# Kernel tuning notes

Measured on AMD Instinct MI355X. Metric: run time of the kernel, lower is better.

## Reference

```python
import jax, jax.numpy as jnp
import numpy as np

B, S, H, DFF, HOP = 64, 512, 512, 2048, 6
THRESHOLD = 1.0 - 0.1  # self.threshold in the torch module


def setup_inputs() -> dict:
    key = jax.random.key(0)
    k = jax.random.split(key, 8)
    sc = 0.02
    return {
        "state": jax.random.normal(k[0], (B, S, H), jnp.float32),
        "inputs": jax.random.normal(k[1], (B, S, H), jnp.float32),
        "time_enc": jax.random.normal(k[2], (1, S, H), jnp.float32) * sc,
        "pos_enc": jax.random.normal(k[3], (1, HOP, H), jnp.float32) * sc,
        "w_p": jax.random.normal(k[4], (H,), jnp.float32) * sc,
        "b_p": jnp.ones((1,), jnp.float32),  # p.bias.data.fill_(1)
        "w1": jax.random.normal(k[5], (H, DFF), jnp.float32) * sc,
        "b1": jnp.zeros((DFF,), jnp.float32),
        "w2": jax.random.normal(k[6], (DFF, H), jnp.float32) * sc,
        "b2": jnp.zeros((H,), jnp.float32),
        "max_hop": HOP,
    }


def reference(state, inputs, time_enc, pos_enc, w_p, b_p, w1, b1, w2, b2, max_hop):
    Bv, Sv, Hv = inputs.shape
    dt = state.dtype
    zeros_bs = jnp.zeros((Bv, Sv), dt)

    def step(carry, pos_t):
        st, halting, remainders, n_updates, prev = carry
        # time + per-step positional signal
        st = st + time_enc[:, :Sv, :] + pos_t[None, None, :]
        # halting probability p = sigmoid(Linear(state)) -> [B,S]
        p = jax.nn.sigmoid(jnp.einsum('bsh,h->bs', st, w_p) + b_p[0])
        still = (halting < 1.0).astype(dt)
        cand = halting + p * still
        new_halted = (cand > THRESHOLD).astype(dt) * still
        still = (cand <= THRESHOLD).astype(dt) * still
        halting = halting + p * still
        remainders = remainders + new_halted * (1.0 - halting)
        halting = halting + new_halted * remainders
        n_updates = n_updates + still + new_halted
        uw = (p * still + new_halted * remainders)[..., None]  # update weights
        # fn(state): wrapped transformer sublayer, here a dense FFN
        st = jnp.maximum(st @ w1 + b1, 0.0) @ w2 + b2
        prev = st * uw + prev * (1.0 - uw)
        return (st, halting, remainders, n_updates, prev), None

    init = (state, zeros_bs, zeros_bs, zeros_bs, jnp.zeros_like(inputs))
    # Fixed max_hop iterations: once a position halts, still/new_halted are 0
    # and all its bookkeeping + blended state are exact no-ops, so this matches
    # the data-dependent torch while-loop exactly.
    (st, halting, remainders, n_updates, prev), _ = jax.lax.scan(
        step, init, pos_enc[0, :max_hop])
    return prev, remainders, n_updates
```

## Files before the change

kernel.cpp:

```cpp
#include <hip/hip_runtime.h>
#include <math.h>

typedef short short8 __attribute__((ext_vector_type(8)));
typedef _Float16 half8 __attribute__((ext_vector_type(8)));
typedef float floatx4 __attribute__((ext_vector_type(4)));

#define Bb 64
#define Ss 512
#define Hh 512
#define DFF 2048
#define HOPS 6
#define BS (Bb*Ss)
#define PS 1048576
#define BUFSZ 16384
#define RSCALE 2048.0f
#define RINV   (1.0f/2048.0f)

__device__ inline unsigned short f16u(float v) {
  _Float16 h = (_Float16)v;
  union { _Float16 h; unsigned short u; } c; c.h = h; return c.u;
}
__device__ inline void split8_store1(const float* xs, unsigned short* dst) {
  unsigned q[4];
#pragma unroll
  for (int j = 0; j < 4; ++j)
    q[j] = (unsigned)f16u(xs[2*j]) | ((unsigned)f16u(xs[2*j+1]) << 16);
  *(int4*)dst = make_int4(q[0], q[1], q[2], q[3]);
}

__device__ __forceinline__ void gload16(const void* g, void* l) {
  __builtin_amdgcn_global_load_lds(
      (const __attribute__((address_space(1))) void*)g,
      (__attribute__((address_space(3))) void*)l, 16, 0, 0);
}

__global__ __launch_bounds__(256) void prep_kernel(
    const float* __restrict__ w, unsigned short* __restrict__ wf,
    int K32, int NTOT, int N)
{
  int id = blockIdx.x * 256 + threadIdx.x;
  if (id >= K32 * NTOT * 64) return;
  int l  = id & 63;
  int NT = (id >> 6) % NTOT;
  int k0 = id / (64 * NTOT);
  int n  = NT * 16 + (l & 15);
  int kb = k0 * 32 + 8 * (l >> 4);
  float xs[8];
#pragma unroll
  for (int j = 0; j < 8; ++j) xs[j] = w[(size_t)(kb + j) * N + n];
  split8_store1(xs, wf + (size_t)id * 8);
}

__global__ __launch_bounds__(1024) void compact_kernel(
    const float* __restrict__ halting, int* __restrict__ idx,
    int* __restrict__ cnt, int tzero)
{
  __shared__ int wsum[16];
  __shared__ int wbase[16];
  __shared__ int s_base;
  int tid = threadIdx.x;
  int lane = tid & 63, wid = tid >> 6;
  int pos = blockIdx.x * 1024 + tid;
  int flag = tzero ? 1 : ((halting[pos] < 1.0f) ? 1 : 0);
  unsigned long long m = __ballot(flag);
  int pre = __popcll(m & ((1ull << lane) - 1ull));
  if (lane == 0) wsum[wid] = __popcll(m);
  __syncthreads();
  if (tid == 0) {
    int a = 0;
#pragma unroll
    for (int i = 0; i < 16; ++i) { wbase[i] = a; a += wsum[i]; }
    s_base = (a > 0) ? atomicAdd(cnt, a) : 0;
  }
  __syncthreads();
  if (flag) idx[s_base + wbase[wid] + pre] = pos;
}

__global__ __launch_bounds__(256) void halt_kernel(
    const float* __restrict__ st, const float* __restrict__ te,
    const float* __restrict__ pe_t, const float* __restrict__ wp,
    const float* __restrict__ bp, float* __restrict__ halting,
    float* __restrict__ remainders, float* __restrict__ n_updates,
    float* __restrict__ uw_c, const int* __restrict__ idxbuf,
    const int* __restrict__ cntp, int tzero)
{
  int cnt = *cntp;
  int i = blockIdx.x * 4 + (threadIdx.x >> 6);
  if (i >= cnt) return;
  int lane = threadIdx.x & 63;
  int pos = idxbuf[i];
  int s = pos & (Ss - 1);
  const float4* stv = (const float4*)(st + (size_t)pos * Hh);
  const float4* tev = (const float4*)(te + (size_t)s * Hh);
  const float4* pev = (const float4*)pe_t;
  const float4* wpv = (const float4*)wp;
  float sum = 0.f;
#pragma unroll
  for (int j = 0; j < 2; ++j) {
    int idx = lane + j * 64;
    float4 a = stv[idx], b = tev[idx], c = pev[idx], w = wpv[idx];
    sum += (a.x + b.x + c.x) * w.x + (a.y + b.y + c.y) * w.y +
           (a.z + b.z + c.z) * w.z + (a.w + b.w + c.w) * w.w;
  }
#pragma unroll
  for (int off = 32; off > 0; off >>= 1) sum += __shfl_xor(sum, off, 64);
  if (lane == 0) {
    float y = sum + bp[0];
    float p = 1.0f / (1.0f + expf(-y));
    const float THRESH = 1.0f - 0.1f;
    float h0  = tzero ? 0.f : halting[pos];
    float rem = tzero ? 0.f : remainders[pos];
    float nup = tzero ? 0.f : n_updates[pos];
    float still = (h0 < 1.0f) ? 1.f : 0.f;
    float cand  = h0 + p * still;
    float nh  = ((cand >  THRESH) ? 1.f : 0.f) * still;
    float st2 = ((cand <= THRESH) ? 1.f : 0.f) * still;
    h0  += p * st2;
    rem += nh * (1.0f - h0);
    h0  += nh * rem;
    nup += st2 + nh;
    float uwv = p * st2 + nh * rem;
    halting[pos]    = h0;
    remainders[pos] = rem;
    n_updates[pos]  = nup;
    uw_c[i]         = uwv;
  }
}

__global__ __launch_bounds__(256) void stagex_kernel(
    const float* __restrict__ st, const float* __restrict__ te,
    const float* __restrict__ pe_t, unsigned short* __restrict__ xf,
    const int* __restrict__ idxbuf, const int* __restrict__ cntp,
    int m_base, int mrows)
{
  const int K32 = Hh / 32;
  int cnt = *cntp;
  int rel = cnt - m_base;
  if (rel <= 0) return;
  if (rel > mrows) rel = mrows;
  int rows_pad = (rel + 127) & ~127;
  if (rows_pad > mrows) rows_pad = mrows;
  int id = blockIdx.x * 256 + threadIdx.x;
  int l = id & 63;
  int f = id >> 6;
  int mtile = f / K32, k0 = f - mtile * K32;
  if (mtile * 16 >= rows_pad) return;
  int m = m_base + mtile * 16 + (l & 15);
  int mc = (m < cnt) ? m : cnt - 1;
  int pos = idxbuf[mc];
  int kb = k0 * 32 + (l >> 4) * 8;
  const float* ap = st + (size_t)pos * Hh + kb;
  const float* tp = te + (size_t)(pos & (Ss - 1)) * Hh + kb;
  const float* pp = pe_t + kb;
  float4 xa = *(const float4*)ap, xb = *(const float4*)(ap + 4);
  float4 ta = *(const float4*)tp, tb = *(const float4*)(tp + 4);
  float4 pa = *(const float4*)pp, pb = *(const float4*)(pp + 4);
  float xs[8];
  xs[0] = xa.x + ta.x + pa.x; xs[1] = xa.y + ta.y + pa.y;
  xs[2] = xa.z + ta.z + pa.z; xs[3] = xa.w + ta.w + pa.w;
  xs[4] = xb.x + tb.x + pb.x; xs[5] = xb.y + tb.y + pb.y;
  xs[6] = xb.z + tb.z + pb.z; xs[7] = xb.w + tb.w + pb.w;
  split8_store1(xs, xf + ((size_t)f * 64 + l) * 8);
}


#define LSTR 66
__global__ __launch_bounds__(256, 2) void gemm1_kernel(
    const unsigned short* __restrict__ xf, const unsigned short* __restrict__ w1f,
    const float* __restrict__ b1, unsigned short* __restrict__ hf,
    const int* __restrict__ cntp, int m_base)
{
  __shared__ __align__(1024) char stage[3 * BUFSZ];
  const int K32 = Hh / 32, NTOT = DFF / 16;
  int lin = blockIdx.x;
  int gsz = gridDim.x;
  int q = gsz >> 3, r = gsz & 7;
  int xcd = lin & 7, idx0 = lin >> 3;
  int swz = (xcd < r) ? (xcd * (q + 1) + idx0)
                      : (r * (q + 1) + (xcd - r) * q + idx0);
  int strip = swz >> 4;
  int nb    = swz & 15;
  int cnt = *cntp;
  int m0 = strip * 128;
  if (m_base + m0 >= cnt) return;
  int tid = threadIdx.x, lane = tid & 63, w = tid >> 6;
  int wm = w >> 1, wn = w & 1;
  int n0 = nb * 128;
  int mtb0 = m0 >> 4, ntb0 = n0 >> 4;
  char* sptr = stage;

  auto stage_step = [&](int bsel, int kk) {
    unsigned so = (unsigned)bsel * (unsigned)BUFSZ;
#pragma unroll
    for (int j = 0; j < 4; ++j) {
      int u = w * 4 + j;
      if (u < 8) {
        const unsigned short* g =
            xf + ((size_t)(mtb0 + u) * K32 + kk) * 512 + (size_t)lane * 8;
        gload16(g, sptr + so + (unsigned)u * 1024u);
      } else {
        int v = u - 8;
        const unsigned short* g =
            w1f + ((size_t)kk * NTOT + (ntb0 + v)) * 512 + (size_t)lane * 8;
        gload16(g, sptr + so + 8192u + (unsigned)v * 1024u);
      }
    }
  };

  floatx4 am[4][4];
#pragma unroll
  for (int i = 0; i < 4; ++i)
#pragma unroll
    for (int j = 0; j < 4; ++j) am[i][j] = (floatx4){0.f, 0.f, 0.f, 0.f};

  stage_step(0, 0);
  int cur = 0;
  for (int k0 = 0; k0 < K32; ++k0) {
    int nxt = (cur == 2) ? 0 : cur + 1;
    if (k0 + 1 < K32) {
      stage_step(nxt, k0 + 1);
      asm volatile("s_waitcnt vmcnt(4)" ::: "memory");
    } else {
      asm volatile("s_waitcnt vmcnt(0)" ::: "memory");
    }
    __builtin_amdgcn_s_barrier();
    asm volatile("" ::: "memory");
    const char* sb = sptr + cur * BUFSZ + (size_t)lane * 16;
    half8 af[4], bf[4];
#pragma unroll
    for (int mt = 0; mt < 4; ++mt)
      af[mt] = *(const half8*)(sb + (wm * 4 + mt) * 1024);
#pragma unroll
    for (int nt = 0; nt < 4; ++nt)
      bf[nt] = *(const half8*)(sb + 8192 + (wn * 4 + nt) * 1024);
    __builtin_amdgcn_s_setprio(1);
#pragma unroll
    for (int mt = 0; mt < 4; ++mt)
#pragma unroll
      for (int nt = 0; nt < 4; ++nt)
        am[mt][nt] = __builtin_amdgcn_mfma_f32_16x16x32_f16(af[mt], bf[nt],
                                                            am[mt][nt], 0, 0, 0);
    __builtin_amdgcn_s_setprio(0);
    asm volatile("" ::: "memory");
    cur = nxt;
  }
  __syncthreads();
  {
    int r0 = (lane >> 4) * 4;
    int c0l = lane & 15;
    int mtb = mtb0 + wm * 4;
    int k2b = (n0 >> 5) + wn * 2;
    float* L = (float*)(void*)sptr + (size_t)w * (16 * LSTR);
    float bias[4];
#pragma unroll
    for (int nt = 0; nt < 4; ++nt) bias[nt] = b1[n0 + wn * 64 + nt * 16 + c0l];
#pragma unroll
    for (int mt = 0; mt < 4; ++mt) {
#pragma unroll
      for (int nt = 0; nt < 4; ++nt)
#pragma unroll
        for (int reg = 0; reg < 4; ++reg)
          L[(r0 + reg) * LSTR + nt * 16 + c0l] =
              fmaxf(am[mt][nt][reg] + bias[nt], 0.f);
#pragma unroll
      for (int k2 = 0; k2 < 2; ++k2) {
        const float* rp = L + (lane & 15) * LSTR + k2 * 32 + (lane >> 4) * 8;
        float xs[8];
        float4 xa = *(const float4*)rp, xb = *(const float4*)(rp + 4);
        xs[0]=xa.x; xs[1]=xa.y; xs[2]=xa.z; xs[3]=xa.w;
        xs[4]=xb.x; xs[5]=xb.y; xs[6]=xb.z; xs[7]=xb.w;
        size_t f2 = (size_t)(mtb + mt) * 64 + (k2b + k2);
        split8_store1(xs, hf + (f2 * 64 + lane) * 8);
      }
    }
  }
}

__global__ __launch_bounds__(256, 2) void gemm2f_kernel(
    const unsigned short* __restrict__ hf, const unsigned short* __restrict__ w2f,
    const float* __restrict__ b2, const float* __restrict__ uw_c,
    float* __restrict__ st_out, float* __restrict__ prev,
    const int* __restrict__ idxbuf, const int* __restrict__ cntp,
    int m_base, int tzero)
{
  __shared__ __align__(1024) char stage[3 * BUFSZ];
  const int K32 = DFF / 32, NTOT = Hh / 16;
  int lin = blockIdx.x;
  int gsz = gridDim.x;
  int q = gsz >> 3, r = gsz & 7;
  int xcd = lin & 7, idx0 = lin >> 3;
  int swz = (xcd < r) ? (xcd * (q + 1) + idx0)
                      : (r * (q + 1) + (xcd - r) * q + idx0);
  int strip = swz >> 2, nb = swz & 3;
  int cnt = *cntp;
  int m0 = strip * 128;
  if (m_base + m0 >= cnt) return;
  int n0 = nb * 128;
  int tid = threadIdx.x, lane = tid & 63, w = tid >> 6;
  int wm = w >> 1, wn = w & 1;
  int mtb0 = m0 >> 4, ntb0 = n0 >> 4;
  char* sptr = stage;

  auto stage_step = [&](int bsel, int kk) {
    unsigned so = (unsigned)bsel * (unsigned)BUFSZ;
#pragma unroll
    for (int j = 0; j < 4; ++j) {
      int u = w * 4 + j;
      if (u < 8) {
        const unsigned short* g =
            hf + ((size_t)(mtb0 + u) * K32 + kk) * 512 + (size_t)lane * 8;
        gload16(g, sptr + so + (unsigned)u * 1024u);
      } else {
        int v = u - 8;
        const unsigned short* g =
            w2f + ((size_t)kk * NTOT + (ntb0 + v)) * 512 + (size_t)lane * 8;
        gload16(g, sptr + so + 8192u + (unsigned)v * 1024u);
      }
    }
  };

  floatx4 am[4][4];
#pragma unroll
  for (int i = 0; i < 4; ++i)
#pragma unroll
    for (int j = 0; j < 4; ++j) am[i][j] = (floatx4){0.f, 0.f, 0.f, 0.f};

  stage_step(0, 0);
  int cur = 0;
  for (int k0 = 0; k0 < K32; ++k0) {
    int nxt = (cur == 2) ? 0 : cur + 1;
    if (k0 + 1 < K32) {
      stage_step(nxt, k0 + 1);
      asm volatile("s_waitcnt vmcnt(4)" ::: "memory");
    } else {
      asm volatile("s_waitcnt vmcnt(0)" ::: "memory");
    }
    __builtin_amdgcn_s_barrier();
    asm volatile("" ::: "memory");
    const char* sb = sptr + cur * BUFSZ + (size_t)lane * 16;
    half8 af[4], bf[4];
#pragma unroll
    for (int mt = 0; mt < 4; ++mt)
      af[mt] = *(const half8*)(sb + (wm * 4 + mt) * 1024);
#pragma unroll
    for (int nt = 0; nt < 4; ++nt)
      bf[nt] = *(const half8*)(sb + 8192 + (wn * 4 + nt) * 1024);
#pragma unroll
    for (int mt = 0; mt < 4; ++mt)
#pragma unroll
      for (int nt = 0; nt < 4; ++nt)
        am[mt][nt] = __builtin_amdgcn_mfma_f32_16x16x32_f16(af[mt], bf[nt],
                                                            am[mt][nt], 0, 0, 0);
    asm volatile("" ::: "memory");
    cur = nxt;
  }
  {
    int r0 = (lane >> 4) * 4;
    int c0l = lane & 15;
    int mtb = mtb0 + wm * 4;
    int njb = ntb0 + wn * 4;
    float bias[4];
#pragma unroll
    for (int nt = 0; nt < 4; ++nt) bias[nt] = b2[(njb + nt) * 16 + c0l];
#pragma unroll
    for (int mt = 0; mt < 4; ++mt) {
      int pos4[4]; float uw4[4]; bool ok4[4];
#pragma unroll
      for (int reg = 0; reg < 4; ++reg) {
        int m = m_base + (mtb + mt) * 16 + r0 + reg;
        ok4[reg] = (m < cnt);
        int mc = ok4[reg] ? m : 0;
        pos4[reg] = idxbuf[mc];
        uw4[reg]  = uw_c[mc];
      }
#pragma unroll
      for (int nt = 0; nt < 4; ++nt) {
        int col = (njb + nt) * 16 + c0l;
#pragma unroll
        for (int reg = 0; reg < 4; ++reg) {
          if (ok4[reg]) {
            float sv = am[mt][nt][reg] + bias[nt];
            size_t off = (size_t)pos4[reg] * Hh + col;
            float pv = tzero ? 0.f : prev[off];
            st_out[off] = sv;
            prev[off] = sv * uw4[reg] + pv * (1.f - uw4[reg]);
          }
        }
      }
    }
  }
}

extern "C" void kernel_launch(void* const* d_in, const int* in_sizes, int n_in,
                              void* d_out, int out_size, void* d_ws, size_t ws_size,
                              hipStream_t stream) {
  const float* state  = (const float*)d_in[0];
  const float* te     = (const float*)d_in[2];
  const float* pe     = (const float*)d_in[3];
  const float* wp     = (const float*)d_in[4];
  const float* bp     = (const float*)d_in[5];
  const float* w1     = (const float*)d_in[6];
  const float* b1     = (const float*)d_in[7];
  const float* w2     = (const float*)d_in[8];
  const float* b2     = (const float*)d_in[9];

  float* out        = (float*)d_out;
  float* prev       = out;
  float* remainders = out + (size_t)BS * Hh;
  float* n_updates  = remainders + BS;

  float*          st      = (float*)d_ws;
  float*          halting = st + (size_t)BS * Hh;
  float*          uw_c    = halting + BS;
  int*            idxbuf  = (int*)(uw_c + BS);
  int*            cntp    = idxbuf + BS;
  unsigned short* w1f     = (unsigned short*)(cntp + 64);
  unsigned short* w2f     = w1f + (size_t)PS;
  unsigned short* hf      = w2f + (size_t)PS;

  size_t fixed = (size_t)((char*)hf - (char*)d_ws);
  size_t avail = (ws_size > fixed) ? (ws_size - fixed) : 0;
  int hrows = (int)((avail / 5120) & ~(size_t)127);
  if (hrows > BS) hrows = BS;
  if (hrows < 128) hrows = 128;
  unsigned short* xf = hf + (size_t)hrows * DFF;
  int nst = hrows / 128;

  hipMemsetAsync(cntp, 0, 64 * sizeof(int), stream);

  prep_kernel<<<512, 256, 0, stream>>>(w1, w1f, Hh / 32, DFF / 16, DFF);
  prep_kernel<<<512, 256, 0, stream>>>(w2, w2f, DFF / 32, Hh / 16, Hh);

  for (int t = 0; t < HOPS; ++t) {
    const float* pe_t = pe + (size_t)t * Hh;
    int* cnt_t = cntp + t;
    int tz = (t == 0) ? 1 : 0;
    const float* st_src = tz ? state : st;
    compact_kernel<<<BS / 1024, 1024, 0, stream>>>(halting, idxbuf, cnt_t, tz);
    halt_kernel<<<BS / 4, 256, 0, stream>>>(st_src, te, pe_t, wp, bp, halting,
                                            remainders, n_updates, uw_c,
                                            idxbuf, cnt_t, tz);
    for (int mb = 0; mb < BS; mb += hrows) {
      stagex_kernel<<<hrows / 4, 256, 0, stream>>>(st_src, te, pe_t, xf, idxbuf,
                                                   cnt_t, mb, hrows);
      gemm1_kernel<<<nst * 16, 256, 0, stream>>>(xf, w1f, b1, hf, cnt_t, mb);
      gemm2f_kernel<<<nst * 4, 256, 0, stream>>>(hf, w2f, b2, uw_c, st, prev,
                                                 idxbuf, cnt_t, mb, tz);
    }
  }
}
```

Measured before the change: 590.2 us.

## Load GEMM B fragments directly to registers and shrink LDS staging

Both GEMM kernels stop staging the weight (B) tiles through LDS. Each wave now loads its B fragments straight from global memory into double-buffered registers, while only the A tile goes through the triple-buffered LDS ring. LDS per block is halved and launch bounds are raised to allow three blocks per CU, aiming at higher occupancy and less LDS traffic. The cost is that B tiles shared across waves are loaded redundantly from global/L2, and register pressure rises under the tighter occupancy bound.

```diff
diff --git a/kernel.cpp b/kernel.cpp
--- a/kernel.cpp
+++ b/kernel.cpp
@@ -12,9 +12,7 @@
 #define HOPS 6
 #define BS (Bb*Ss)
 #define PS 1048576
-#define BUFSZ 16384
-#define RSCALE 2048.0f
-#define RINV   (1.0f/2048.0f)
+#define BUFA 8192
 
 __device__ inline unsigned short f16u(float v) {
   _Float16 h = (_Float16)v;
@@ -165,12 +163,12 @@
 
 
 #define LSTR 66
-__global__ __launch_bounds__(256, 2) void gemm1_kernel(
+__global__ __launch_bounds__(256, 3) void gemm1_kernel(
     const unsigned short* __restrict__ xf, const unsigned short* __restrict__ w1f,
     const float* __restrict__ b1, unsigned short* __restrict__ hf,
     const int* __restrict__ cntp, int m_base)
 {
-  __shared__ __align__(1024) char stage[3 * BUFSZ];
+  __shared__ __align__(1024) char stage[3 * BUFA];
   const int K32 = Hh / 32, NTOT = DFF / 16;
   int lin = blockIdx.x;
   int gsz = gridDim.x;
@@ -189,22 +187,21 @@
   int mtb0 = m0 >> 4, ntb0 = n0 >> 4;
   char* sptr = stage;
 
-  auto stage_step = [&](int bsel, int kk) {
-    unsigned so = (unsigned)bsel * (unsigned)BUFSZ;
-#pragma unroll
-    for (int j = 0; j < 4; ++j) {
-      int u = w * 4 + j;
-      if (u < 8) {
-        const unsigned short* g =
-            xf + ((size_t)(mtb0 + u) * K32 + kk) * 512 + (size_t)lane * 8;
-        gload16(g, sptr + so + (unsigned)u * 1024u);
-      } else {
-        int v = u - 8;
-        const unsigned short* g =
-            w1f + ((size_t)kk * NTOT + (ntb0 + v)) * 512 + (size_t)lane * 8;
-        gload16(g, sptr + so + 8192u + (unsigned)v * 1024u);
-      }
-    }
+  auto stageA = [&](int bsel, int kk) {
+    unsigned so = (unsigned)bsel * (unsigned)BUFA;
+#pragma unroll
+    for (int j = 0; j < 2; ++j) {
+      int u = w * 2 + j;
+      const unsigned short* g =
+          xf + ((size_t)(mtb0 + u) * K32 + kk) * 512 + (size_t)lane * 8;
+      gload16(g, sptr + so + (unsigned)u * 1024u);
+    }
+  };
+  auto loadB = [&](half8 (&b)[4], int kk) {
+#pragma unroll
+    for (int nt = 0; nt < 4; ++nt)
+      b[nt] = *(const half8*)(w1f +
+          ((size_t)kk * NTOT + (ntb0 + wn * 4 + nt)) * 512 + (size_t)lane * 8);
   };
 
   floatx4 am[4][4];
@@ -213,36 +210,42 @@
 #pragma unroll
     for (int j = 0; j < 4; ++j) am[i][j] = (floatx4){0.f, 0.f, 0.f, 0.f};
 
-  stage_step(0, 0);
-  int cur = 0;
-  for (int k0 = 0; k0 < K32; ++k0) {
+  half8 bfA[4], bfB[4];
+  stageA(0, 0);
+  loadB(bfA, 0);
+
+  auto iter = [&](int k, int cur, half8 (&bu)[4], half8 (&bl)[4]) -> int {
     int nxt = (cur == 2) ? 0 : cur + 1;
-    if (k0 + 1 < K32) {
-      stage_step(nxt, k0 + 1);
-      asm volatile("s_waitcnt vmcnt(4)" ::: "memory");
+    if (k + 1 < K32) {
+      stageA(nxt, k + 1);
+      loadB(bl, k + 1);
+      asm volatile("s_waitcnt vmcnt(6)" ::: "memory");
     } else {
       asm volatile("s_waitcnt vmcnt(0)" ::: "memory");
     }
     __builtin_amdgcn_s_barrier();
     asm volatile("" ::: "memory");
-    const char* sb = sptr + cur * BUFSZ + (size_t)lane * 16;
-    half8 af[4], bf[4];
+    const char* sb = sptr + cur * BUFA + (size_t)lane * 16;
+    half8 af[4];
 #pragma unroll
     for (int mt = 0; mt < 4; ++mt)
       af[mt] = *(const half8*)(sb + (wm * 4 + mt) * 1024);
-#pragma unroll
-    for (int nt = 0; nt < 4; ++nt)
-      bf[nt] = *(const half8*)(sb + 8192 + (wn * 4 + nt) * 1024);
     __builtin_amdgcn_s_setprio(1);
 #pragma unroll
     for (int mt = 0; mt < 4; ++mt)
 #pragma unroll
       for (int nt = 0; nt < 4; ++nt)
-        am[mt][nt] = __builtin_amdgcn_mfma_f32_16x16x32_f16(af[mt], bf[nt],
+        am[mt][nt] = __builtin_amdgcn_mfma_f32_16x16x32_f16(af[mt], bu[nt],
                                                             am[mt][nt], 0, 0, 0);
     __builtin_amdgcn_s_setprio(0);
     asm volatile("" ::: "memory");
-    cur = nxt;
+    return nxt;
+  };
+
+  int cur = 0;
+  for (int k0 = 0; k0 < K32; k0 += 2) {
+    cur = iter(k0,     cur, bfA, bfB);
+    cur = iter(k0 + 1, cur, bfB, bfA);
   }
   __syncthreads();
   {
@@ -276,14 +279,14 @@
   }
 }
 
-__global__ __launch_bounds__(256, 2) void gemm2f_kernel(
+__global__ __launch_bounds__(256, 3) void gemm2f_kernel(
     const unsigned short* __restrict__ hf, const unsigned short* __restrict__ w2f,
     const float* __restrict__ b2, const float* __restrict__ uw_c,
     float* __restrict__ st_out, float* __restrict__ prev,
     const int* __restrict__ idxbuf, const int* __restrict__ cntp,
     int m_base, int tzero)
 {
-  __shared__ __align__(1024) char stage[3 * BUFSZ];
+  __shared__ __align__(1024) char stage[3 * BUFA];
   const int K32 = DFF / 32, NTOT = Hh / 16;
   int lin = blockIdx.x;
   int gsz = gridDim.x;
@@ -301,22 +304,21 @@
   int mtb0 = m0 >> 4, ntb0 = n0 >> 4;
   char* sptr = stage;
 
-  auto stage_step = [&](int bsel, int kk) {
-    unsigned so = (unsigned)bsel * (unsigned)BUFSZ;
-#pragma unroll
-    for (int j = 0; j < 4; ++j) {
-      int u = w * 4 + j;
-      if (u < 8) {
-        const unsigned short* g =
-            hf + ((size_t)(mtb0 + u) * K32 + kk) * 512 + (size_t)lane * 8;
-        gload16(g, sptr + so + (unsigned)u * 1024u);
-      } else {
-        int v = u - 8;
-        const unsigned short* g =
-            w2f + ((size_t)kk * NTOT + (ntb0 + v)) * 512 + (size_t)lane * 8;
-        gload16(g, sptr + so + 8192u + (unsigned)v * 1024u);
-      }
-    }
+  auto stageA = [&](int bsel, int kk) {
+    unsigned so = (unsigned)bsel * (unsigned)BUFA;
+#pragma unroll
+    for (int j = 0; j < 2; ++j) {
+      int u = w * 2 + j;
+      const unsigned short* g =
+          hf + ((size_t)(mtb0 + u) * K32 + kk) * 512 + (size_t)lane * 8;
+      gload16(g, sptr + so + (unsigned)u * 1024u);
+    }
+  };
+  auto loadB = [&](half8 (&b)[4], int kk) {
+#pragma unroll
+    for (int nt = 0; nt < 4; ++nt)
+      b[nt] = *(const half8*)(w2f +
+          ((size_t)kk * NTOT + (ntb0 + wn * 4 + nt)) * 512 + (size_t)lane * 8);
   };
 
   floatx4 am[4][4];
@@ -325,34 +327,40 @@
 #pragma unroll
     for (int j = 0; j < 4; ++j) am[i][j] = (floatx4){0.f, 0.f, 0.f, 0.f};
 
-  stage_step(0, 0);
-  int cur = 0;
-  for (int k0 = 0; k0 < K32; ++k0) {
+  half8 bfA[4], bfB[4];
+  stageA(0, 0);
+  loadB(bfA, 0);
+
+  auto iter = [&](int k, int cur, half8 (&bu)[4], half8 (&bl)[4]) -> int {
     int nxt = (cur == 2) ? 0 : cur + 1;
-    if (k0 + 1 < K32) {
-      stage_step(nxt, k0 + 1);
-      asm volatile("s_waitcnt vmcnt(4)" ::: "memory");
+    if (k + 1 < K32) {
+      stageA(nxt, k + 1);
+      loadB(bl, k + 1);
+      asm volatile("s_waitcnt vmcnt(6)" ::: "memory");
     } else {
       asm volatile("s_waitcnt vmcnt(0)" ::: "memory");
     }
     __builtin_amdgcn_s_barrier();
     asm volatile("" ::: "memory");
-    const char* sb = sptr + cur * BUFSZ + (size_t)lane * 16;
-    half8 af[4], bf[4];
+    const char* sb = sptr + cur * BUFA + (size_t)lane * 16;
+    half8 af[4];
 #pragma unroll
     for (int mt = 0; mt < 4; ++mt)
       af[mt] = *(const half8*)(sb + (wm * 4 + mt) * 1024);
 #pragma unroll
-    for (int nt = 0; nt < 4; ++nt)
-      bf[nt] = *(const half8*)(sb + 8192 + (wn * 4 + nt) * 1024);
-#pragma unroll
     for (int mt = 0; mt < 4; ++mt)
 #pragma unroll
       for (int nt = 0; nt < 4; ++nt)
-        am[mt][nt] = __builtin_amdgcn_mfma_f32_16x16x32_f16(af[mt], bf[nt],
+        am[mt][nt] = __builtin_amdgcn_mfma_f32_16x16x32_f16(af[mt], bu[nt],
                                                             am[mt][nt], 0, 0, 0);
     asm volatile("" ::: "memory");
-    cur = nxt;
+    return nxt;
+  };
+
+  int cur = 0;
+  for (int k0 = 0; k0 < K32; k0 += 2) {
+    cur = iter(k0,     cur, bfA, bfB);
+    cur = iter(k0 + 1, cur, bfB, bfA);
   }
   {
     int r0 = (lane >> 4) * 4;
```

Measured after the change: 566.7 us, median of 3. -4.0%, faster.
